# Optimization experiments

Measured on AMD Instinct MI355X. Metric: run time of the kernel, lower is better.

## Reference

```python
import jax, jax.numpy as jnp
import numpy as np

B, T, I, H, O = 128, 256, 64, 1024, 64


def setup_inputs() -> dict:
    key = jax.random.key(0)
    ks = jax.random.split(key, 16)
    s_ih1 = 1.0 / np.sqrt(H)
    def mk(k, shape, s):
        return jax.random.uniform(k, shape, jnp.float32, -s, s)
    return {
        "x": jax.random.normal(ks[0], (B, T, I), jnp.float32),
        # RNNCell 1: input I -> hidden H
        "W_ih1": mk(ks[1], (H, I), s_ih1),
        "b_ih1": mk(ks[2], (H,), s_ih1),
        "W_hh1": mk(ks[3], (H, H), s_ih1),
        "b_hh1": mk(ks[4], (H,), s_ih1),
        # RNNCell 2: hidden H -> hidden H
        "W_ih2": mk(ks[5], (H, H), s_ih1),
        "b_ih2": mk(ks[6], (H,), s_ih1),
        "W_hh2": mk(ks[7], (H, H), s_ih1),
        "b_hh2": mk(ks[8], (H,), s_ih1),
        # gate: 2H -> H
        "Wg": mk(ks[9], (H, 2 * H), 1.0 / np.sqrt(2 * H)),
        "bg": mk(ks[10], (H,), 1.0 / np.sqrt(2 * H)),
        # output heads: H -> O
        "Wo1": mk(ks[11], (O, H), s_ih1),
        "bo1": mk(ks[12], (O,), s_ih1),
        "Wo2": mk(ks[13], (O, H), s_ih1),
        "bo2": mk(ks[14], (O,), s_ih1),
    }


def reference(x, W_ih1, b_ih1, W_hh1, b_hh1, W_ih2, b_ih2, W_hh2, b_hh2,
              Wg, bg, Wo1, bo1, Wo2, bo2):
    batch = x.shape[0]
    h1_0 = jnp.zeros((batch, H), x.dtype)
    h2_0 = jnp.zeros((batch, H), x.dtype)
    u_0 = jnp.ones((batch, H), x.dtype)

    def step(carry, x_t):
        h1, h2, u = carry
        # RNNCell 1
        h1 = jnp.tanh(x_t @ W_ih1.T + b_ih1 + h1 @ W_hh1.T + b_hh1)
        # RNNCell 2, gated convex blend with previous h2
        h2_new = jnp.tanh(h1 @ W_ih2.T + b_ih2 + h2 @ W_hh2.T + b_hh2)
        h2 = u * h2_new + (1.0 - u) * h2
        # dual tanh output head
        out = jnp.tanh(h1 @ Wo1.T + bo1) + jnp.tanh(h2 @ Wo2.T + bo2)
        # gate for NEXT step, computed from current hiddens
        u = jax.nn.sigmoid(jnp.concatenate([h1, h2], axis=1) @ Wg.T + bg)
        return (h1, h2, u), out

    xs = jnp.swapaxes(x, 0, 1)  # [T, B, I]
    _, outs = jax.lax.scan(step, (h1_0, h2_0, u_0), xs)
    return jnp.swapaxes(outs, 0, 1)  # [B, T, O]
```

## Files before the change

### kernel.cpp

```cpp
#include <hip/hip_runtime.h>
#include <cstddef>

using bf16x8 = __attribute__((ext_vector_type(8))) short;
using f32x4  = __attribute__((ext_vector_type(4))) float;

constexpr int Bb = 128;
constexpr int Tt = 256;
constexpr int Hh = 1024;
constexpr int Oo = 64;
constexpr int NBLK = 168;
constexpr int FLAG_STRIDE = 32;
constexpr int RS = 1048;

constexpr int R_H1 = 8;
constexpr int R_H2 = 16;
constexpr int R_P2 = 6;
constexpr int R_PG = 6;
constexpr int R_PO = 16;

constexpr int FH1 = 0;
constexpr int FP2 = 32;
constexpr int FPG = 64;
constexpr int FPO = 96;
constexpr int FH2 = 100;
constexpr int FZO = 164;

__device__ __forceinline__ float bf2f(short s) {
  unsigned int u = ((unsigned int)(unsigned short)s) << 16;
  float f;
  __builtin_memcpy(&f, &u, 4);
  return f;
}
__device__ __forceinline__ short f2bf(float f) {
  unsigned int u;
  __builtin_memcpy(&u, &f, 4);
  u += 0x7fffu + ((u >> 16) & 1u);
  return (short)(u >> 16);
}
__device__ __forceinline__ bf16x8 as_bf(int4 v) {
  union { int4 i; bf16x8 b; } u; u.i = v; return u.b;
}
__device__ __forceinline__ float ldf(const float* p) {
  return __hip_atomic_load((float*)p, __ATOMIC_RELAXED, __HIP_MEMORY_SCOPE_AGENT);
}
__device__ __forceinline__ void stf(float* p, float v) {
  __hip_atomic_store(p, v, __ATOMIC_RELAXED, __HIP_MEMORY_SCOPE_AGENT);
}
__device__ __forceinline__ unsigned ldu(const unsigned* p) {
  return __hip_atomic_load((unsigned*)p, __ATOMIC_RELAXED, __HIP_MEMORY_SCOPE_AGENT);
}

#define LD16A(d, p) asm volatile("global_load_dwordx4 %0, %1, off sc1" \
                                 : "=v"(d) : "v"((const void*)(p)))

__device__ __forceinline__ void stage32(short* As, const short* src, int tid) {
  const int row = tid >> 3;
  const int c0  = (tid & 7) * 8;
  const short* gp = src + (size_t)row * Hh + c0;
  short* lp = As + row * RS + c0;
  int4 r0[8], r1[8];
#pragma unroll
  for (int j = 0; j < 8; ++j) LD16A(r0[j], gp + j * 64);
#pragma unroll
  for (int j = 0; j < 8; ++j) LD16A(r1[j], gp + 512 + j * 64);
  asm volatile("s_waitcnt vmcnt(8)" ::: "memory");
#pragma unroll
  for (int j = 0; j < 8; ++j) *(int4*)(lp + j * 64) = r0[j];
  asm volatile("s_waitcnt vmcnt(0)" ::: "memory");
#pragma unroll
  for (int j = 0; j < 8; ++j) *(int4*)(lp + 512 + j * 64) = r1[j];
}

struct BPre {
  const short *bp0, *bp1;
  int4 b0v[6], b1v[6];
};
__device__ __forceinline__ void prefillB(BPre& P,
    const short* __restrict__ B0, size_t st0,
    const short* __restrict__ B1, size_t st1, int lm, int q) {
  P.bp0 = B0 + (size_t)lm * st0 + q * 8;
  P.bp1 = B1 + (size_t)lm * st1 + q * 8;
#pragma unroll
  for (int c = 0; c < 5; ++c) {
    P.b0v[c] = *(const int4*)(P.bp0 + c * 32);
    P.b1v[c] = *(const int4*)(P.bp1 + c * 32);
  }
}
__device__ __forceinline__ void pass32p(const short* As, int lm, int q,
    BPre& P, f32x4 (&acc)[2][2]) {
  const short* ap0 = As + lm * RS + q * 8;
  const short* ap1 = ap0 + 16 * RS;
#pragma unroll
  for (int c = 0; c < 32; ++c) {
    if (c + 5 < 32) {
      P.b0v[(c + 5) % 6] = *(const int4*)(P.bp0 + (c + 5) * 32);
      P.b1v[(c + 5) % 6] = *(const int4*)(P.bp1 + (c + 5) * 32);
    }
    const bf16x8 a0 = as_bf(*(const int4*)(ap0 + c * 32));
    const bf16x8 a1 = as_bf(*(const int4*)(ap1 + c * 32));
    const bf16x8 b0 = as_bf(P.b0v[c % 6]);
    const bf16x8 b1 = as_bf(P.b1v[c % 6]);
    acc[0][0] = __builtin_amdgcn_mfma_f32_16x16x32_bf16(a0, b0, acc[0][0], 0, 0, 0);
    acc[0][1] = __builtin_amdgcn_mfma_f32_16x16x32_bf16(a1, b0, acc[0][1], 0, 0, 0);
    acc[1][0] = __builtin_amdgcn_mfma_f32_16x16x32_bf16(a0, b1, acc[1][0], 0, 0, 0);
    acc[1][1] = __builtin_amdgcn_mfma_f32_16x16x32_bf16(a1, b1, acc[1][1], 0, 0, 0);
  }
}

__device__ __forceinline__ void poll_ge(const unsigned* flags, int base,
                                        int mask, unsigned gen) {
  const unsigned* f = flags + (size_t)(base + (threadIdx.x & mask)) * FLAG_STRIDE;
  while (!__all(ldu(f) >= gen))
    __builtin_amdgcn_s_sleep(2);
}

#define POST_FLAG(GEN) do {                                                \
    asm volatile("s_waitcnt vmcnt(0) lgkmcnt(0)" ::: "memory");            \
    __syncthreads();                                                       \
    if (tid == 0)                                                          \
      __hip_atomic_store(p.flags + (size_t)bid * FLAG_STRIDE, (unsigned)(GEN), \
                         __ATOMIC_RELAXED, __HIP_MEMORY_SCOPE_AGENT);      \
  } while (0)

#define ST_BF16_PAIR(BASE, ROW, COL, HV) do {                              \
    const int _ov = __shfl_xor((int)(unsigned short)(HV), 1, 64);          \
    if ((lm & 1) == 0) {                                                   \
      const unsigned _pk = (unsigned)(unsigned short)(HV) | ((unsigned)_ov << 16); \
      __hip_atomic_store((unsigned*)((BASE) + (size_t)(ROW) * Hh + (COL)), _pk, \
                         __ATOMIC_RELAXED, __HIP_MEMORY_SCOPE_AGENT);      \
    } } while (0)

struct RP {
  short *h1ring;
  short *h2ring;
  float *h2f;
  float *pre2f;
  float *pg1f;
  float *po1f;
  const short* prex;
  const short *whh1, *wih2, *whh2, *wg, *wo1, *wo2;
  const float *b_ih2, *b_hh2, *bg, *bo1, *bo2;
  float* out;
  unsigned* flags;
};

__global__ void __launch_bounds__(256, 1) rnn_kernel(RP p) {
  __shared__ short As[32 * RS];
  const int tid = threadIdx.x;
  const int lane = tid & 63;
  const int wv = tid >> 6;
  const int lm = lane & 15;
  const int q = lane >> 4;
  const int bid = blockIdx.x;

  int role, mb, cb;
  if      (bid < 32)  { role = 0; mb = (bid >> 3) * 32;         cb = (bid & 7) * 128; }
  else if (bid < 64)  { role = 1; mb = ((bid - 32) >> 3) * 32;  cb = ((bid - 32) & 7) * 128; }
  else if (bid < 96)  { role = 2; mb = ((bid - 64) >> 3) * 32;  cb = ((bid - 64) & 7) * 128; }
  else if (bid < 100) { role = 3; mb = (bid - 96) * 32;         cb = 0; }
  else if (bid < 164) { role = 4; mb = ((bid - 100) >> 4) * 32; cb = ((bid - 100) & 15) * 64; }
  else                { role = 5; mb = (bid - 164) * 32;        cb = 0; }

  int colw;
  if (role == 4) colw = cb + wv * 16;
  else if (role == 3 || role == 5) colw = (wv & 1) * 32;
  else colw = cb + wv * 32;

  float bias0 = 0.f, bias1 = 0.f;
  if (role == 1) {
    bias0 = p.b_ih2[colw + lm] + p.b_hh2[colw + lm];
    bias1 = p.b_ih2[colw + 16 + lm] + p.b_hh2[colw + 16 + lm];
  } else if (role == 2) {
    bias0 = p.bg[colw + lm]; bias1 = p.bg[colw + 16 + lm];
  } else if (role == 3) {
    bias0 = p.bo1[colw + lm]; bias1 = p.bo1[colw + 16 + lm];
  } else if (role == 5) {
    bias0 = p.bo2[colw + lm]; bias1 = p.bo2[colw + 16 + lm];
  }

  const short* B0; const short* B1;
  size_t st0 = Hh, st1 = Hh;
  if      (role == 0) { B0 = p.whh1 + (size_t)colw * Hh; B1 = p.whh1 + (size_t)(colw + 16) * Hh; }
  else if (role == 1) { B0 = p.wih2 + (size_t)colw * Hh; B1 = p.wih2 + (size_t)(colw + 16) * Hh; }
  else if (role == 2) { B0 = p.wg + (size_t)colw * (2 * Hh); B1 = p.wg + (size_t)(colw + 16) * (2 * Hh); st0 = st1 = 2 * Hh; }
  else if (role == 3) { B0 = p.wo1 + (size_t)colw * Hh; B1 = p.wo1 + (size_t)(colw + 16) * Hh; }
  else if (role == 4) { B0 = p.whh2 + (size_t)colw * Hh; B1 = p.wg + Hh + (size_t)colw * (2 * Hh); st1 = 2 * Hh; }
  else                { B0 = p.wo2 + (size_t)colw * Hh; B1 = p.wo2 + (size_t)(colw + 16) * Hh; }

  const size_t HS = (size_t)Bb * Hh;
  const f32x4 z4 = {0.f, 0.f, 0.f, 0.f};

  if (role == 0) {
    for (int t = 0; t < Tt; ++t) {
      BPre P; prefillB(P, B0, st0, B1, st1, lm, q);
      short prs[2][2][4];
      const short* pr = p.prex + (size_t)t * HS;
#pragma unroll
      for (int n = 0; n < 2; ++n)
#pragma unroll
        for (int rf = 0; rf < 2; ++rf)
#pragma unroll
          for (int r = 0; r < 4; ++r)
            prs[n][rf][r] = pr[(size_t)(mb + rf * 16 + q * 4 + r) * Hh + colw + n * 16 + lm];
      if (tid < 64) {
        if (t >= 1) poll_ge(p.flags, FH1, 31, (unsigned)t);
        if (t >= 8) {
          poll_ge(p.flags, FP2, 31, (unsigned)(t - 7));
          poll_ge(p.flags, FPG, 31, (unsigned)(t - 7));
          poll_ge(p.flags, FPO, 3,  (unsigned)(t - 7));
        }
      }
      __syncthreads();
      const short* h1prev = p.h1ring + (size_t)((t + R_H1 - 1) % R_H1) * HS;
      stage32(As, h1prev + (size_t)mb * Hh, tid);
      __syncthreads();
      f32x4 acc[2][2]; acc[0][0] = acc[0][1] = acc[1][0] = acc[1][1] = z4;
      pass32p(As, lm, q, P, acc);
      short* h1out = p.h1ring + (size_t)(t % R_H1) * HS;
#pragma unroll
      for (int n = 0; n < 2; ++n)
#pragma unroll
        for (int rf = 0; rf < 2; ++rf)
#pragma unroll
          for (int r = 0; r < 4; ++r) {
            const int row = mb + rf * 16 + q * 4 + r;
            const int col = colw + n * 16 + lm;
            const short hv = f2bf(tanhf(acc[n][rf][r] + bf2f(prs[n][rf][r])));
            ST_BF16_PAIR(h1out, row, col, hv);
          }
      POST_FLAG(t + 1);
    }
  } else if (role == 1) {
    for (int t = 0; t < Tt; ++t) {
      BPre P; prefillB(P, B0, st0, B1, st1, lm, q);
      if (tid < 64) {
        poll_ge(p.flags, FH1, 31, (unsigned)(t + 1));
        if (t >= R_P2) poll_ge(p.flags, FH2, 63, (unsigned)(t - 5));
      }
      __syncthreads();
      const short* h1cur = p.h1ring + (size_t)(t % R_H1) * HS;
      stage32(As, h1cur + (size_t)mb * Hh, tid);
      __syncthreads();
      f32x4 acc[2][2]; acc[0][0] = acc[0][1] = acc[1][0] = acc[1][1] = z4;
      pass32p(As, lm, q, P, acc);
      float* dst = p.pre2f + (size_t)(t % R_P2) * HS;
#pragma unroll
      for (int n = 0; n < 2; ++n)
#pragma unroll
        for (int rf = 0; rf < 2; ++rf)
#pragma unroll
          for (int r = 0; r < 4; ++r) {
            const int row = mb + rf * 16 + q * 4 + r;
            const int col = colw + n * 16 + lm;
            stf(dst + (size_t)row * Hh + col, acc[n][rf][r] + (n ? bias1 : bias0));
          }
      POST_FLAG(t + 1);
    }
  } else if (role == 2) {
    for (int t = 0; t < Tt; ++t) {
      BPre P; prefillB(P, B0, st0, B1, st1, lm, q);
      if (tid < 64) {
        poll_ge(p.flags, FH1, 31, (unsigned)(t + 1));
        if (t >= R_PG) poll_ge(p.flags, FH2, 63, (unsigned)(t - 4));
      }
      __syncthreads();
      const short* h1cur = p.h1ring + (size_t)(t % R_H1) * HS;
      stage32(As, h1cur + (size_t)mb * Hh, tid);
      __syncthreads();
      f32x4 acc[2][2]; acc[0][0] = acc[0][1] = acc[1][0] = acc[1][1] = z4;
      pass32p(As, lm, q, P, acc);
      float* dst = p.pg1f + (size_t)(t % R_PG) * HS;
#pragma unroll
      for (int n = 0; n < 2; ++n)
#pragma unroll
        for (int rf = 0; rf < 2; ++rf)
#pragma unroll
          for (int r = 0; r < 4; ++r) {
            const int row = mb + rf * 16 + q * 4 + r;
            const int col = colw + n * 16 + lm;
            stf(dst + (size_t)row * Hh + col, acc[n][rf][r] + (n ? bias1 : bias0));
          }
      POST_FLAG(t + 1);
    }
  } else if (role == 3) {
    for (int t = 0; t < Tt; ++t) {
      BPre P;
      if (wv < 2) prefillB(P, B0, st0, B1, st1, lm, q);
      if (tid < 64) {
        poll_ge(p.flags, FH1, 31, (unsigned)(t + 1));
        if (t >= R_PO) poll_ge(p.flags, FZO, 3, (unsigned)(t - 15));
      }
      __syncthreads();
      const short* h1cur = p.h1ring + (size_t)(t % R_H1) * HS;
      stage32(As, h1cur + (size_t)mb * Hh, tid);
      __syncthreads();
      if (wv < 2) {
        f32x4 acc[2][2]; acc[0][0] = acc[0][1] = acc[1][0] = acc[1][1] = z4;
        pass32p(As, lm, q, P, acc);
        float* dst = p.po1f + (size_t)(t % R_PO) * (Bb * Oo);
#pragma unroll
        for (int n = 0; n < 2; ++n)
#pragma unroll
          for (int rf = 0; rf < 2; ++rf)
#pragma unroll
            for (int r = 0; r < 4; ++r) {
              const int row = mb + rf * 16 + q * 4 + r;
              const int col = colw + n * 16 + lm;
              stf(dst + (size_t)row * Oo + col,
                  tanhf(acc[n][rf][r] + (n ? bias1 : bias0)));
            }
      }
      POST_FLAG(t + 1);
    }
  } else if (role == 4) {
    for (int s = 0; s < Tt; ++s) {
      BPre P; prefillB(P, B0, st0, B1, st1, lm, q);
      if (tid < 64) {
        poll_ge(p.flags, FP2, 31, (unsigned)(s + 1));
        if (s >= 1) {
          poll_ge(p.flags, FPG, 31, (unsigned)s);
          poll_ge(p.flags, FH2, 63, (unsigned)s);
        }
        if (s >= R_H2) poll_ge(p.flags, FZO, 3, (unsigned)(s - 15));
      }
      __syncthreads();
      float p2v[2][4], pg1v[2][4], hpv[2][4];
      const float* pre2s = p.pre2f + (size_t)(s % R_P2) * HS;
      const float* pg1s  = p.pg1f + (size_t)((s + R_PG - 1) % R_PG) * HS;
#pragma unroll
      for (int rf = 0; rf < 2; ++rf)
#pragma unroll
        for (int r = 0; r < 4; ++r) {
          const size_t idx = (size_t)(mb + rf * 16 + q * 4 + r) * Hh + colw + lm;
          p2v[rf][r] = ldf(pre2s + idx);
          pg1v[rf][r] = (s > 0) ? ldf(pg1s + idx) : 0.f;
          hpv[rf][r] = p.h2f[idx];
        }
      const short* h2prev = p.h2ring + (size_t)((s + R_H2 - 1) % R_H2) * HS;
      stage32(As, h2prev + (size_t)mb * Hh, tid);
      __syncthreads();
      f32x4 acc[2][2]; acc[0][0] = acc[0][1] = acc[1][0] = acc[1][1] = z4;
      pass32p(As, lm, q, P, acc);
      short* h2out = p.h2ring + (size_t)(s % R_H2) * HS;
#pragma unroll
      for (int rf = 0; rf < 2; ++rf)
#pragma unroll
        for (int r = 0; r < 4; ++r) {
          const int row = mb + rf * 16 + q * 4 + r;
          const int col = colw + lm;
          const size_t idx = (size_t)row * Hh + col;
          const float u = (s == 0) ? 1.f
              : 1.f / (1.f + expf(-(acc[1][rf][r] + pg1v[rf][r])));
          const float hn = tanhf(acc[0][rf][r] + p2v[rf][r]);
          const float nv = fmaf(u, hn - hpv[rf][r], hpv[rf][r]);
          p.h2f[idx] = nv;
          const short hv = f2bf(nv);
          ST_BF16_PAIR(h2out, row, col, hv);
        }
      POST_FLAG(s + 1);
    }
  } else {
    for (int ot = 0; ot < Tt; ++ot) {
      BPre P;
      if (wv < 2) prefillB(P, B0, st0, B1, st1, lm, q);
      if (tid < 64) {
        poll_ge(p.flags, FH2, 63, (unsigned)(ot + 1));
        poll_ge(p.flags, FPO, 3,  (unsigned)(ot + 1));
      }
      __syncthreads();
      const float* po1s = p.po1f + (size_t)(ot % R_PO) * (Bb * Oo);
      float pv[2][2][4];
      if (wv < 2) {
#pragma unroll
        for (int n = 0; n < 2; ++n)
#pragma unroll
          for (int rf = 0; rf < 2; ++rf)
#pragma unroll
            for (int r = 0; r < 4; ++r)
              pv[n][rf][r] = ldf(po1s + (size_t)(mb + rf * 16 + q * 4 + r) * Oo
                                 + colw + n * 16 + lm);
      }
      const short* h2cur = p.h2ring + (size_t)(ot % R_H2) * HS;
      stage32(As, h2cur + (size_t)mb * Hh, tid);
      __syncthreads();
      if (wv < 2) {
        f32x4 acc[2][2]; acc[0][0] = acc[0][1] = acc[1][0] = acc[1][1] = z4;
        pass32p(As, lm, q, P, acc);
#pragma unroll
        for (int n = 0; n < 2; ++n)
#pragma unroll
          for (int rf = 0; rf < 2; ++rf)
#pragma unroll
            for (int r = 0; r < 4; ++r) {
              const int row = mb + rf * 16 + q * 4 + r;
              const int col = colw + n * 16 + lm;
              p.out[(size_t)row * (Tt * Oo) + (size_t)ot * Oo + col] =
                  pv[n][rf][r] + tanhf(acc[n][rf][r] + (n ? bias1 : bias0));
            }
      }
      POST_FLAG(ot + 1);
    }
  }
}

__global__ void __launch_bounds__(256) prex_kernel(
    const float* __restrict__ x, const float* __restrict__ wih1,
    const float* __restrict__ b_ih1, const float* __restrict__ b_hh1,
    short* __restrict__ prex) {
  const int tid = threadIdx.x;
  const int lane = tid & 63;
  const int wv = tid >> 6;
  const int lm = lane & 15;
  const int q = lane >> 4;
  const int bm = blockIdx.x >> 4;
  const int bn = blockIdx.x & 15;
  const int rowbase = bm * 64;
  const int col = bn * 64 + wv * 16 + lm;

  const f32x4 z4 = {0.f, 0.f, 0.f, 0.f};
  f32x4 acc[4];
#pragma unroll
  for (int mt = 0; mt < 4; ++mt) acc[mt] = z4;

#pragma unroll
  for (int kc = 0; kc < 2; ++kc) {
    const float* bp = wih1 + col * 64 + kc * 32 + q * 8;
    bf16x8 bf;
#pragma unroll
    for (int j = 0; j < 8; ++j) bf[j] = f2bf(bp[j]);
#pragma unroll
    for (int mt = 0; mt < 4; ++mt) {
      const float* ap = x + (size_t)(rowbase + mt * 16 + lm) * 64 + kc * 32 + q * 8;
      bf16x8 af;
#pragma unroll
      for (int j = 0; j < 8; ++j) af[j] = f2bf(ap[j]);
      acc[mt] = __builtin_amdgcn_mfma_f32_16x16x32_bf16(af, bf, acc[mt], 0, 0, 0);
    }
  }
  const float bia = b_ih1[col] + b_hh1[col];
#pragma unroll
  for (int mt = 0; mt < 4; ++mt) {
#pragma unroll
    for (int r = 0; r < 4; ++r) {
      const int row = rowbase + mt * 16 + q * 4 + r;
      const int b  = row >> 8;
      const int tt = row & 255;
      prex[((size_t)tt * Bb + b) * Hh + col] = f2bf(acc[mt][r] + bia);
    }
  }
}

__global__ void conv_kernel(const float* __restrict__ s, short* __restrict__ d, int n) {
  int i = blockIdx.x * blockDim.x + threadIdx.x;
  const int stride = gridDim.x * blockDim.x;
  for (; i < n; i += stride) d[i] = f2bf(s[i]);
}

__global__ void init_kernel(short* h1ring, short* h2ring,
                            float* h2f, unsigned* flags) {
  const int i = blockIdx.x * blockDim.x + threadIdx.x;
  const size_t HS = (size_t)Bb * Hh;
  h1ring[(size_t)(R_H1 - 1) * HS + i] = 0;
  h2ring[(size_t)(R_H2 - 1) * HS + i] = 0;
  h2f[i] = 0.f;
  if (i < 256) flags[i * FLAG_STRIDE] = 0u;
}

extern "C" void kernel_launch(void* const* d_in, const int* in_sizes, int n_in,
                              void* d_out, int out_size, void* d_ws, size_t ws_size,
                              hipStream_t stream) {
  (void)in_sizes; (void)n_in; (void)out_size; (void)ws_size;
  const float* x      = (const float*)d_in[0];
  const float* W_ih1  = (const float*)d_in[1];
  const float* b_ih1  = (const float*)d_in[2];
  const float* W_hh1  = (const float*)d_in[3];
  const float* b_hh1  = (const float*)d_in[4];
  const float* W_ih2  = (const float*)d_in[5];
  const float* b_ih2  = (const float*)d_in[6];
  const float* W_hh2  = (const float*)d_in[7];
  const float* b_hh2  = (const float*)d_in[8];
  const float* Wg     = (const float*)d_in[9];
  const float* bg     = (const float*)d_in[10];
  const float* Wo1    = (const float*)d_in[11];
  const float* bo1    = (const float*)d_in[12];
  const float* Wo2    = (const float*)d_in[13];
  const float* bo2    = (const float*)d_in[14];

  char* ws = (char*)d_ws;
  size_t off = 0;
  auto alloc = [&](size_t bytes) -> void* {
    void* ptr = ws + off;
    off += (bytes + 255) & ~(size_t)255;
    return ptr;
  };
  short* whh1 = (short*)alloc((size_t)Hh * Hh * 2);
  short* wih2 = (short*)alloc((size_t)Hh * Hh * 2);
  short* whh2 = (short*)alloc((size_t)Hh * Hh * 2);
  short* wg   = (short*)alloc((size_t)Hh * 2 * Hh * 2);
  short* wo1  = (short*)alloc((size_t)Oo * Hh * 2);
  short* wo2  = (short*)alloc((size_t)Oo * Hh * 2);
  short* prex = (short*)alloc((size_t)Bb * Tt * Hh * 2);
  short* h1ring = (short*)alloc((size_t)R_H1 * Bb * Hh * 2);
  short* h2ring = (short*)alloc((size_t)R_H2 * Bb * Hh * 2);
  float* h2f  = (float*)alloc((size_t)Bb * Hh * 4);
  float* pre2f= (float*)alloc((size_t)R_P2 * Bb * Hh * 4);
  float* pg1f = (float*)alloc((size_t)R_PG * Bb * Hh * 4);
  float* po1f = (float*)alloc((size_t)R_PO * Bb * Oo * 4);
  unsigned* flags = (unsigned*)alloc(256 * FLAG_STRIDE * 4);

  conv_kernel<<<1024, 256, 0, stream>>>(W_hh1, whh1, Hh * Hh);
  conv_kernel<<<1024, 256, 0, stream>>>(W_ih2, wih2, Hh * Hh);
  conv_kernel<<<1024, 256, 0, stream>>>(W_hh2, whh2, Hh * Hh);
  conv_kernel<<<2048, 256, 0, stream>>>(Wg,    wg,   Hh * 2 * Hh);
  conv_kernel<<<256,  256, 0, stream>>>(Wo1,   wo1,  Oo * Hh);
  conv_kernel<<<256,  256, 0, stream>>>(Wo2,   wo2,  Oo * Hh);
  init_kernel<<<512, 256, 0, stream>>>(h1ring, h2ring, h2f, flags);
  prex_kernel<<<8192, 256, 0, stream>>>(x, W_ih1, b_ih1, b_hh1, prex);

  RP p;
  p.h1ring = h1ring; p.h2ring = h2ring;
  p.h2f = h2f; p.pre2f = pre2f; p.pg1f = pg1f; p.po1f = po1f;
  p.prex = prex;
  p.whh1 = whh1; p.wih2 = wih2; p.whh2 = whh2;
  p.wg = wg; p.wo1 = wo1; p.wo2 = wo2;
  p.b_ih2 = b_ih2; p.b_hh2 = b_hh2;
  p.bg = bg; p.bo1 = bo1; p.bo2 = bo2;
  p.out = (float*)d_out;
  p.flags = flags;

  rnn_kernel<<<NBLK, 256, 0, stream>>>(p);
}
```

Before: 3.117 ms.

## Merge pre2 and gate roles, widen h2 tiles, and use per-row-group flag dependencies

Folds the two h1-consuming roles (W_ih2 and the h1 half of Wg) into one block group that computes four weight stripes per pass, so both products reuse one staging of h1 from LDS. The h2 role now covers 128 columns per block with four stripes instead of 64. This cuts the persistent grid from 168 to 104 blocks. Polling is narrowed from global all-block waits to the specific row-group flags each block depends on, which shortens the cross-block synchronisation chain per timestep. In exchange each block does twice the MFMA work per step and holds more registers for the four-stripe prefetch, which can lengthen the per-step critical path.

```diff
diff --git a/kernel.cpp b/kernel.cpp
--- a/kernel.cpp
+++ b/kernel.cpp
@@ -8,22 +8,20 @@
 constexpr int Tt = 256;
 constexpr int Hh = 1024;
 constexpr int Oo = 64;
-constexpr int NBLK = 168;
+constexpr int NBLK = 104;
 constexpr int FLAG_STRIDE = 32;
 constexpr int RS = 1048;
 
 constexpr int R_H1 = 8;
 constexpr int R_H2 = 16;
-constexpr int R_P2 = 6;
-constexpr int R_PG = 6;
+constexpr int R_PP = 6;
 constexpr int R_PO = 16;
 
 constexpr int FH1 = 0;
-constexpr int FP2 = 32;
-constexpr int FPG = 64;
-constexpr int FPO = 96;
-constexpr int FH2 = 100;
-constexpr int FZO = 164;
+constexpr int FPH = 32;
+constexpr int FPO = 64;
+constexpr int FH2 = 68;
+constexpr int FZO = 100;
 
 __device__ __forceinline__ float bf2f(short s) {
   unsigned int u = ((unsigned int)(unsigned short)s) << 16;
@@ -104,6 +102,45 @@
     acc[0][1] = __builtin_amdgcn_mfma_f32_16x16x32_bf16(a1, b0, acc[0][1], 0, 0, 0);
     acc[1][0] = __builtin_amdgcn_mfma_f32_16x16x32_bf16(a0, b1, acc[1][0], 0, 0, 0);
     acc[1][1] = __builtin_amdgcn_mfma_f32_16x16x32_bf16(a1, b1, acc[1][1], 0, 0, 0);
+  }
+}
+
+struct BPre4 {
+  const short* bp[4];
+  int4 bv[4][4];
+};
+__device__ __forceinline__ void prefillB4(BPre4& P,
+    const short* B0, size_t st0, const short* B1, size_t st1,
+    const short* B2, size_t st2, const short* B3, size_t st3, int lm, int q) {
+  P.bp[0] = B0 + (size_t)lm * st0 + q * 8;
+  P.bp[1] = B1 + (size_t)lm * st1 + q * 8;
+  P.bp[2] = B2 + (size_t)lm * st2 + q * 8;
+  P.bp[3] = B3 + (size_t)lm * st3 + q * 8;
+#pragma unroll
+  for (int c = 0; c < 3; ++c)
+#pragma unroll
+    for (int s = 0; s < 4; ++s)
+      P.bv[s][c] = *(const int4*)(P.bp[s] + c * 32);
+}
+__device__ __forceinline__ void pass32q(const short* As, int lm, int q,
+    BPre4& P, f32x4 (&acc)[4][2]) {
+  const short* ap0 = As + lm * RS + q * 8;
+  const short* ap1 = ap0 + 16 * RS;
+#pragma unroll
+  for (int c = 0; c < 32; ++c) {
+    if (c + 3 < 32) {
+#pragma unroll
+      for (int s = 0; s < 4; ++s)
+        P.bv[s][(c + 3) & 3] = *(const int4*)(P.bp[s] + (c + 3) * 32);
+    }
+    const bf16x8 a0 = as_bf(*(const int4*)(ap0 + c * 32));
+    const bf16x8 a1 = as_bf(*(const int4*)(ap1 + c * 32));
+#pragma unroll
+    for (int s = 0; s < 4; ++s) {
+      const bf16x8 b = as_bf(P.bv[s][c & 3]);
+      acc[s][0] = __builtin_amdgcn_mfma_f32_16x16x32_bf16(a0, b, acc[s][0], 0, 0, 0);
+      acc[s][1] = __builtin_amdgcn_mfma_f32_16x16x32_bf16(a1, b, acc[s][1], 0, 0, 0);
+    }
   }
 }
 
@@ -153,46 +190,17 @@
   const int q = lane >> 4;
   const int bid = blockIdx.x;
 
-  int role, mb, cb;
-  if      (bid < 32)  { role = 0; mb = (bid >> 3) * 32;         cb = (bid & 7) * 128; }
-  else if (bid < 64)  { role = 1; mb = ((bid - 32) >> 3) * 32;  cb = ((bid - 32) & 7) * 128; }
-  else if (bid < 96)  { role = 2; mb = ((bid - 64) >> 3) * 32;  cb = ((bid - 64) & 7) * 128; }
-  else if (bid < 100) { role = 3; mb = (bid - 96) * 32;         cb = 0; }
-  else if (bid < 164) { role = 4; mb = ((bid - 100) >> 4) * 32; cb = ((bid - 100) & 15) * 64; }
-  else                { role = 5; mb = (bid - 164) * 32;        cb = 0; }
-
-  int colw;
-  if (role == 4) colw = cb + wv * 16;
-  else if (role == 3 || role == 5) colw = (wv & 1) * 32;
-  else colw = cb + wv * 32;
-
-  float bias0 = 0.f, bias1 = 0.f;
-  if (role == 1) {
-    bias0 = p.b_ih2[colw + lm] + p.b_hh2[colw + lm];
-    bias1 = p.b_ih2[colw + 16 + lm] + p.b_hh2[colw + 16 + lm];
-  } else if (role == 2) {
-    bias0 = p.bg[colw + lm]; bias1 = p.bg[colw + 16 + lm];
-  } else if (role == 3) {
-    bias0 = p.bo1[colw + lm]; bias1 = p.bo1[colw + 16 + lm];
-  } else if (role == 5) {
-    bias0 = p.bo2[colw + lm]; bias1 = p.bo2[colw + 16 + lm];
-  }
-
-  const short* B0; const short* B1;
-  size_t st0 = Hh, st1 = Hh;
-  if      (role == 0) { B0 = p.whh1 + (size_t)colw * Hh; B1 = p.whh1 + (size_t)(colw + 16) * Hh; }
-  else if (role == 1) { B0 = p.wih2 + (size_t)colw * Hh; B1 = p.wih2 + (size_t)(colw + 16) * Hh; }
-  else if (role == 2) { B0 = p.wg + (size_t)colw * (2 * Hh); B1 = p.wg + (size_t)(colw + 16) * (2 * Hh); st0 = st1 = 2 * Hh; }
-  else if (role == 3) { B0 = p.wo1 + (size_t)colw * Hh; B1 = p.wo1 + (size_t)(colw + 16) * Hh; }
-  else if (role == 4) { B0 = p.whh2 + (size_t)colw * Hh; B1 = p.wg + Hh + (size_t)colw * (2 * Hh); st1 = 2 * Hh; }
-  else                { B0 = p.wo2 + (size_t)colw * Hh; B1 = p.wo2 + (size_t)(colw + 16) * Hh; }
-
   const size_t HS = (size_t)Bb * Hh;
   const f32x4 z4 = {0.f, 0.f, 0.f, 0.f};
 
-  if (role == 0) {
+  if (bid < 32) {
+    const int g = bid, gm = g >> 3;
+    const int mb = gm * 32, cb = (g & 7) * 128;
+    const int colw = cb + wv * 32;
+    const short* B0 = p.whh1 + (size_t)colw * Hh;
+    const short* B1 = p.whh1 + (size_t)(colw + 16) * Hh;
     for (int t = 0; t < Tt; ++t) {
-      BPre P; prefillB(P, B0, st0, B1, st1, lm, q);
+      BPre P; prefillB(P, B0, Hh, B1, Hh, lm, q);
       short prs[2][2][4];
       const short* pr = p.prex + (size_t)t * HS;
 #pragma unroll
@@ -203,11 +211,10 @@
           for (int r = 0; r < 4; ++r)
             prs[n][rf][r] = pr[(size_t)(mb + rf * 16 + q * 4 + r) * Hh + colw + n * 16 + lm];
       if (tid < 64) {
-        if (t >= 1) poll_ge(p.flags, FH1, 31, (unsigned)t);
+        if (t >= 1) poll_ge(p.flags, FH1 + gm * 8, 7, (unsigned)t);
         if (t >= 8) {
-          poll_ge(p.flags, FP2, 31, (unsigned)(t - 7));
-          poll_ge(p.flags, FPG, 31, (unsigned)(t - 7));
-          poll_ge(p.flags, FPO, 3,  (unsigned)(t - 7));
+          poll_ge(p.flags, FPH + gm * 8, 7, (unsigned)(t - 7));
+          poll_ge(p.flags, FPO + gm, 0, (unsigned)(t - 7));
         }
       }
       __syncthreads();
@@ -230,20 +237,34 @@
           }
       POST_FLAG(t + 1);
     }
-  } else if (role == 1) {
+  } else if (bid < 64) {
+    const int g = bid - 32, gm = g >> 3;
+    const int mb = gm * 32, cb = (g & 7) * 128;
+    const int colw = cb + wv * 32;
+    const float b20 = p.b_ih2[colw + lm] + p.b_hh2[colw + lm];
+    const float b21 = p.b_ih2[colw + 16 + lm] + p.b_hh2[colw + 16 + lm];
+    const float bg0 = p.bg[colw + lm];
+    const float bg1 = p.bg[colw + 16 + lm];
     for (int t = 0; t < Tt; ++t) {
-      BPre P; prefillB(P, B0, st0, B1, st1, lm, q);
+      BPre4 P;
+      prefillB4(P, p.wih2 + (size_t)colw * Hh, Hh,
+                   p.wih2 + (size_t)(colw + 16) * Hh, Hh,
+                   p.wg + (size_t)colw * (2 * Hh), 2 * Hh,
+                   p.wg + (size_t)(colw + 16) * (2 * Hh), 2 * Hh, lm, q);
       if (tid < 64) {
-        poll_ge(p.flags, FH1, 31, (unsigned)(t + 1));
-        if (t >= R_P2) poll_ge(p.flags, FH2, 63, (unsigned)(t - 5));
+        poll_ge(p.flags, FH1 + gm * 8, 7, (unsigned)(t + 1));
+        if (t >= R_PP) poll_ge(p.flags, FH2 + g, 0, (unsigned)(t - 4));
       }
       __syncthreads();
       const short* h1cur = p.h1ring + (size_t)(t % R_H1) * HS;
       stage32(As, h1cur + (size_t)mb * Hh, tid);
       __syncthreads();
-      f32x4 acc[2][2]; acc[0][0] = acc[0][1] = acc[1][0] = acc[1][1] = z4;
-      pass32p(As, lm, q, P, acc);
-      float* dst = p.pre2f + (size_t)(t % R_P2) * HS;
+      f32x4 acc[4][2];
+#pragma unroll
+      for (int s = 0; s < 4; ++s) acc[s][0] = acc[s][1] = z4;
+      pass32q(As, lm, q, P, acc);
+      float* d2 = p.pre2f + (size_t)(t % R_PP) * HS;
+      float* dg = p.pg1f + (size_t)(t % R_PP) * HS;
 #pragma unroll
       for (int n = 0; n < 2; ++n)
 #pragma unroll
@@ -252,43 +273,25 @@
           for (int r = 0; r < 4; ++r) {
             const int row = mb + rf * 16 + q * 4 + r;
             const int col = colw + n * 16 + lm;
-            stf(dst + (size_t)row * Hh + col, acc[n][rf][r] + (n ? bias1 : bias0));
+            stf(d2 + (size_t)row * Hh + col, acc[n][rf][r] + (n ? b21 : b20));
+            stf(dg + (size_t)row * Hh + col, acc[2 + n][rf][r] + (n ? bg1 : bg0));
           }
       POST_FLAG(t + 1);
     }
-  } else if (role == 2) {
-    for (int t = 0; t < Tt; ++t) {
-      BPre P; prefillB(P, B0, st0, B1, st1, lm, q);
-      if (tid < 64) {
-        poll_ge(p.flags, FH1, 31, (unsigned)(t + 1));
-        if (t >= R_PG) poll_ge(p.flags, FH2, 63, (unsigned)(t - 4));
-      }
-      __syncthreads();
-      const short* h1cur = p.h1ring + (size_t)(t % R_H1) * HS;
-      stage32(As, h1cur + (size_t)mb * Hh, tid);
-      __syncthreads();
-      f32x4 acc[2][2]; acc[0][0] = acc[0][1] = acc[1][0] = acc[1][1] = z4;
-      pass32p(As, lm, q, P, acc);
-      float* dst = p.pg1f + (size_t)(t % R_PG) * HS;
-#pragma unroll
-      for (int n = 0; n < 2; ++n)
-#pragma unroll
-        for (int rf = 0; rf < 2; ++rf)
-#pragma unroll
-          for (int r = 0; r < 4; ++r) {
-            const int row = mb + rf * 16 + q * 4 + r;
-            const int col = colw + n * 16 + lm;
-            stf(dst + (size_t)row * Hh + col, acc[n][rf][r] + (n ? bias1 : bias0));
-          }
-      POST_FLAG(t + 1);
-    }
-  } else if (role == 3) {
+  } else if (bid < 68) {
+    const int g = bid - 64;
+    const int mb = g * 32;
+    const int colw = (wv & 1) * 32;
+    const float b0 = p.bo1[colw + lm];
+    const float b1 = p.bo1[colw + 16 + lm];
+    const short* B0 = p.wo1 + (size_t)colw * Hh;
+    const short* B1 = p.wo1 + (size_t)(colw + 16) * Hh;
     for (int t = 0; t < Tt; ++t) {
       BPre P;
-      if (wv < 2) prefillB(P, B0, st0, B1, st1, lm, q);
+      if (wv < 2) prefillB(P, B0, Hh, B1, Hh, lm, q);
       if (tid < 64) {
-        poll_ge(p.flags, FH1, 31, (unsigned)(t + 1));
-        if (t >= R_PO) poll_ge(p.flags, FZO, 3, (unsigned)(t - 15));
+        poll_ge(p.flags, FH1 + g * 8, 7, (unsigned)(t + 1));
+        if (t >= R_PO) poll_ge(p.flags, FZO + g, 0, (unsigned)(t - 15));
       }
       __syncthreads();
       const short* h1cur = p.h1ring + (size_t)(t % R_H1) * HS;
@@ -307,65 +310,82 @@
               const int row = mb + rf * 16 + q * 4 + r;
               const int col = colw + n * 16 + lm;
               stf(dst + (size_t)row * Oo + col,
-                  tanhf(acc[n][rf][r] + (n ? bias1 : bias0)));
+                  tanhf(acc[n][rf][r] + (n ? b1 : b0)));
             }
       }
       POST_FLAG(t + 1);
     }
-  } else if (role == 4) {
+  } else if (bid < 100) {
+    const int g = bid - 68, gm = g >> 3;
+    const int mb = gm * 32, cb = (g & 7) * 128;
+    const int colw = cb + wv * 32;
     for (int s = 0; s < Tt; ++s) {
-      BPre P; prefillB(P, B0, st0, B1, st1, lm, q);
+      BPre4 P;
+      prefillB4(P, p.whh2 + (size_t)colw * Hh, Hh,
+                   p.whh2 + (size_t)(colw + 16) * Hh, Hh,
+                   p.wg + Hh + (size_t)colw * (2 * Hh), 2 * Hh,
+                   p.wg + Hh + (size_t)(colw + 16) * (2 * Hh), 2 * Hh, lm, q);
       if (tid < 64) {
-        poll_ge(p.flags, FP2, 31, (unsigned)(s + 1));
-        if (s >= 1) {
-          poll_ge(p.flags, FPG, 31, (unsigned)s);
-          poll_ge(p.flags, FH2, 63, (unsigned)s);
-        }
-        if (s >= R_H2) poll_ge(p.flags, FZO, 3, (unsigned)(s - 15));
-      }
-      __syncthreads();
-      float p2v[2][4], pg1v[2][4], hpv[2][4];
-      const float* pre2s = p.pre2f + (size_t)(s % R_P2) * HS;
-      const float* pg1s  = p.pg1f + (size_t)((s + R_PG - 1) % R_PG) * HS;
-#pragma unroll
-      for (int rf = 0; rf < 2; ++rf)
-#pragma unroll
-        for (int r = 0; r < 4; ++r) {
-          const size_t idx = (size_t)(mb + rf * 16 + q * 4 + r) * Hh + colw + lm;
-          p2v[rf][r] = ldf(pre2s + idx);
-          pg1v[rf][r] = (s > 0) ? ldf(pg1s + idx) : 0.f;
-          hpv[rf][r] = p.h2f[idx];
-        }
+        poll_ge(p.flags, FPH + g, 0, (unsigned)(s + 1));
+        if (s >= 1) poll_ge(p.flags, FH2 + gm * 8, 7, (unsigned)s);
+        if (s >= R_H2) poll_ge(p.flags, FZO + gm, 0, (unsigned)(s - 15));
+      }
+      __syncthreads();
+      float p2v[2][2][4], pg1v[2][2][4], hpv[2][2][4];
+      const float* pre2s = p.pre2f + (size_t)(s % R_PP) * HS;
+      const float* pg1s  = p.pg1f + (size_t)((s + R_PP - 1) % R_PP) * HS;
+#pragma unroll
+      for (int n = 0; n < 2; ++n)
+#pragma unroll
+        for (int rf = 0; rf < 2; ++rf)
+#pragma unroll
+          for (int r = 0; r < 4; ++r) {
+            const size_t idx = (size_t)(mb + rf * 16 + q * 4 + r) * Hh + colw + n * 16 + lm;
+            p2v[n][rf][r] = ldf(pre2s + idx);
+            pg1v[n][rf][r] = (s > 0) ? ldf(pg1s + idx) : 0.f;
+            hpv[n][rf][r] = p.h2f[idx];
+          }
       const short* h2prev = p.h2ring + (size_t)((s + R_H2 - 1) % R_H2) * HS;
       stage32(As, h2prev + (size_t)mb * Hh, tid);
       __syncthreads();
-      f32x4 acc[2][2]; acc[0][0] = acc[0][1] = acc[1][0] = acc[1][1] = z4;
-      pass32p(As, lm, q, P, acc);
+      f32x4 acc[4][2];
+#pragma unroll
+      for (int st = 0; st < 4; ++st) acc[st][0] = acc[st][1] = z4;
+      pass32q(As, lm, q, P, acc);
       short* h2out = p.h2ring + (size_t)(s % R_H2) * HS;
 #pragma unroll
-      for (int rf = 0; rf < 2; ++rf)
-#pragma unroll
-        for (int r = 0; r < 4; ++r) {
-          const int row = mb + rf * 16 + q * 4 + r;
-          const int col = colw + lm;
-          const size_t idx = (size_t)row * Hh + col;
-          const float u = (s == 0) ? 1.f
-              : 1.f / (1.f + expf(-(acc[1][rf][r] + pg1v[rf][r])));
-          const float hn = tanhf(acc[0][rf][r] + p2v[rf][r]);
-          const float nv = fmaf(u, hn - hpv[rf][r], hpv[rf][r]);
-          p.h2f[idx] = nv;
-          const short hv = f2bf(nv);
-          ST_BF16_PAIR(h2out, row, col, hv);
-        }
+      for (int n = 0; n < 2; ++n)
+#pragma unroll
+        for (int rf = 0; rf < 2; ++rf)
+#pragma unroll
+          for (int r = 0; r < 4; ++r) {
+            const int row = mb + rf * 16 + q * 4 + r;
+            const int col = colw + n * 16 + lm;
+            const size_t idx = (size_t)row * Hh + col;
+            const float u = (s == 0) ? 1.f
+                : 1.f / (1.f + expf(-(acc[2 + n][rf][r] + pg1v[n][rf][r])));
+            const float hn = tanhf(acc[n][rf][r] + p2v[n][rf][r]);
+            const float nv = fmaf(u, hn - hpv[n][rf][r], hpv[n][rf][r]);
+            p.h2f[idx] = nv;
+            const short hv = f2bf(nv);
+            ST_BF16_PAIR(h2out, row, col, hv);
+          }
       POST_FLAG(s + 1);
     }
   } else {
+    const int g = bid - 100;
+    const int mb = g * 32;
+    const int colw = (wv & 1) * 32;
+    const float b0 = p.bo2[colw + lm];
+    const float b1 = p.bo2[colw + 16 + lm];
+    const short* B0 = p.wo2 + (size_t)colw * Hh;
+    const short* B1 = p.wo2 + (size_t)(colw + 16) * Hh;
     for (int ot = 0; ot < Tt; ++ot) {
       BPre P;
-      if (wv < 2) prefillB(P, B0, st0, B1, st1, lm, q);
+      if (wv < 2) prefillB(P, B0, Hh, B1, Hh, lm, q);
       if (tid < 64) {
-        poll_ge(p.flags, FH2, 63, (unsigned)(ot + 1));
-        poll_ge(p.flags, FPO, 3,  (unsigned)(ot + 1));
+        poll_ge(p.flags, FH2 + g * 8, 7, (unsigned)(ot + 1));
+        poll_ge(p.flags, FPO + g, 0, (unsigned)(ot + 1));
       }
       __syncthreads();
       const float* po1s = p.po1f + (size_t)(ot % R_PO) * (Bb * Oo);
@@ -395,7 +415,7 @@
               const int row = mb + rf * 16 + q * 4 + r;
               const int col = colw + n * 16 + lm;
               p.out[(size_t)row * (Tt * Oo) + (size_t)ot * Oo + col] =
-                  pv[n][rf][r] + tanhf(acc[n][rf][r] + (n ? bias1 : bias0));
+                  pv[n][rf][r] + tanhf(acc[n][rf][r] + (n ? b1 : b0));
             }
       }
       POST_FLAG(ot + 1);
@@ -503,8 +523,8 @@
   short* h1ring = (short*)alloc((size_t)R_H1 * Bb * Hh * 2);
   short* h2ring = (short*)alloc((size_t)R_H2 * Bb * Hh * 2);
   float* h2f  = (float*)alloc((size_t)Bb * Hh * 4);
-  float* pre2f= (float*)alloc((size_t)R_P2 * Bb * Hh * 4);
-  float* pg1f = (float*)alloc((size_t)R_PG * Bb * Hh * 4);
+  float* pre2f= (float*)alloc((size_t)R_PP * Bb * Hh * 4);
+  float* pg1f = (float*)alloc((size_t)R_PP * Bb * Hh * 4);
   float* po1f = (float*)alloc((size_t)R_PO * Bb * Oo * 4);
   unsigned* flags = (unsigned*)alloc(256 * FLAG_STRIDE * 4);
 
```

New measurement: 5.302 ms. 70.1% more time.
